# Kernel tuning notes

Measured on AMD Instinct MI355X. Metric: run time of the kernel, lower is better.

Reference implementation:

```python
import jax, jax.numpy as jnp
import numpy as np

WS = 8            # window_size
SHIFT = WS // 2   # cyclic shift for 'SW' type
HEAD_DIM = 32

def _rel_index(ws):
    # pairwise relative coordinate indices within a window, offset to [0, 2ws-2]
    cord = np.array([[i, j] for i in range(ws) for j in range(ws)])
    rel = cord[:, None, :] - cord[None, :, :] + ws - 1
    return rel[:, :, 0], rel[:, :, 1]

def _shift_mask(h_w, w_w, p):
    # boolean attention mask for shifted windows; True = masked (-inf)
    s = p - SHIFT
    m = np.zeros((h_w, w_w, p, p, p, p), dtype=bool)
    m[-1, :, :s, :, s:, :] = True
    m[-1, :, s:, :, :s, :] = True
    m[:, -1, :, :s, :, s:] = True
    m[:, -1, :, s:, :, :s] = True
    return m.reshape(h_w * w_w, p * p, p * p)

def setup_inputs() -> dict:
    key = jax.random.key(0)
    ks = jax.random.split(key, 6)
    b, H, W, c = 4, 256, 256, 256
    nh = c // HEAD_DIM
    return {
        "x": jax.random.normal(ks[0], (b, H, W, c), jnp.float32),
        "W_qkv": jax.random.normal(ks[1], (c, 3 * c), jnp.float32) * 0.02,
        "b_qkv": jnp.zeros((3 * c,), jnp.float32),
        "rel_pos": jax.random.normal(ks[2], (nh, 2 * WS - 1, 2 * WS - 1), jnp.float32) * 0.02,
        "W_out": jax.random.normal(ks[3], (c, c), jnp.float32) * 0.02,
        "b_out": jnp.zeros((c,), jnp.float32),
    }

def reference(x, W_qkv, b_qkv, rel_pos, W_out, b_out):
    b, H, W, c = x.shape
    nh = c // HEAD_DIM
    scale = HEAD_DIM ** -0.5
    # cyclic shift (type == 'SW')
    x = jnp.roll(x, (-SHIFT, -SHIFT), axis=(1, 2))
    hw, ww = H // WS, W // WS
    nw, p2 = hw * ww, WS * WS
    # partition into windows: [b, nw, p2, c]
    xw = x.reshape(b, hw, WS, ww, WS, c).transpose(0, 1, 3, 2, 4, 5).reshape(b, nw, p2, c)
    # QKV projection; layout of out dim is (3, n_heads, head_dim)
    qkv = (xw @ W_qkv + b_qkv).reshape(b, nw, p2, 3, nh, HEAD_DIM)
    q, k, v = qkv[..., 0, :, :], qkv[..., 1, :, :], qkv[..., 2, :, :]
    # attention scores per head/window: [h, b, nw, p2, p2]
    sim = jnp.einsum('bwphc,bwqhc->hbwpq', q, k) * scale
    ri, rj = _rel_index(WS)
    sim = sim + rel_pos[:, ri, rj][:, None, None]            # relative position bias
    mask = jnp.asarray(_shift_mask(hw, ww, WS))              # [nw, p2, p2]
    sim = jnp.where(mask[None, None], -jnp.inf, sim)
    probs = jax.nn.softmax(sim, axis=-1)
    out = jnp.einsum('hbwpq,bwqhc->bwphc', probs, v).reshape(b, nw, p2, nh * HEAD_DIM)
    out = out @ W_out + b_out
    # un-window: [b, H, W, c_out]
    out = out.reshape(b, hw, ww, WS, WS, -1).transpose(0, 1, 3, 2, 4, 5).reshape(b, H, W, -1)
    return jnp.roll(out, (SHIFT, SHIFT), axis=(1, 2))
```

## Files before the change

kernel.cpp:

```cpp
#include <hip/hip_runtime.h>
#include <hip/hip_bf16.h>

typedef __attribute__((ext_vector_type(4))) float f32x4;
typedef __attribute__((ext_vector_type(2))) unsigned int u32x2;
typedef __attribute__((ext_vector_type(8))) short s16x8;
typedef __attribute__((ext_vector_type(8))) __bf16 bf16v8;
typedef __attribute__((ext_vector_type(8))) _Float16 f16v8;

#define LDS_XS 0
#define LDS_QS 32768
#define LDS_KS 65536
#define LDS_VT 98304
#define LDS_PR 131072
#define LDS_TOT 147456

__device__ __forceinline__ f32x4 mfma16(s16x8 a, s16x8 b, f32x4 c) {
  return __builtin_amdgcn_mfma_f32_16x16x32_bf16(
      __builtin_bit_cast(bf16v8, a), __builtin_bit_cast(bf16v8, b), c, 0, 0, 0);
}
__device__ __forceinline__ f32x4 mfma16h(s16x8 a, s16x8 b, f32x4 c) {
  return __builtin_amdgcn_mfma_f32_16x16x32_f16(
      __builtin_bit_cast(f16v8, a), __builtin_bit_cast(f16v8, b), c, 0, 0, 0);
}

__device__ __forceinline__ unsigned int cvt2(float a, float b) {
  __hip_bfloat162 r = __float22bfloat162_rn(make_float2(a, b));
  unsigned int u;
  __builtin_memcpy(&u, &r, 4);
  return u;
}
__device__ __forceinline__ unsigned int cvt2h(float a, float b) {
  auto r = __builtin_amdgcn_cvt_pkrtz(a, b);
  unsigned int u;
  __builtin_memcpy(&u, &r, 4);
  return u;
}

__device__ __forceinline__ short f2bf(float f) {
  unsigned u = __float_as_uint(f);
  u += 0x7fffu + ((u >> 16) & 1u);
  return (short)(u >> 16);
}

__device__ __forceinline__ int swz512(int row, int colByte) {
  return row * 512 + (colByte ^ ((row & 7) << 4));
}
__device__ __forceinline__ int swz128(int row, int colByte) {
  return row * 128 + (colByte ^ ((row & 7) << 4));
}

__global__ void prep_w(const float* __restrict__ Wqkv, const float* __restrict__ Wout,
                       const float* __restrict__ relp,
                       short* __restrict__ wqkvT, short* __restrict__ wH,
                       float* __restrict__ relt) {
  int t = blockIdx.x * 256 + threadIdx.x;
  if (t < 768 * 256) {
    int n = t >> 8, k = t & 255;
    wqkvT[t] = f2bf(Wqkv[k * 768 + n]);
  } else if (t < 768 * 256 + 256 * 256) {
    int t2 = t - 768 * 256;
    int n = t2 >> 8, k = t2 & 255;
    _Float16 h = (_Float16)Wout[k * 256 + n];
    unsigned short us;
    __builtin_memcpy(&us, &h, 2);
    wH[t2] = (short)us;
  } else {
    int u = t - 768 * 256 - 256 * 256;
    int r = u & 3, l = (u >> 2) & 63, strip = (u >> 8) & 3;
    int qt = (u >> 10) & 3, h = (u >> 12) & 7, var = (u >> 15) & 3;
    int p = strip * 16 + (l & 15);
    int q = qt * 16 + ((l >> 4) << 2) + r;
    int pi = p >> 3, pj = p & 7, qi = q >> 3, qj = q & 7;
    bool mrow = (var >> 1) & 1, mcol = var & 1;
    bool mk = (mrow && ((pi < 4) != (qi < 4))) || (mcol && ((pj < 4) != (qj < 4)));
    relt[u] = mk ? -1e30f : relp[h * 225 + (pi - qi + 7) * 15 + (pj - qj + 7)];
  }
}

__global__ __launch_bounds__(512, 2) void swin_mfma(
    const float* __restrict__ x, const float* __restrict__ bqkv,
    const float* __restrict__ bout,
    const short* __restrict__ wqkvT, const short* __restrict__ wH,
    const float* __restrict__ relt, float* __restrict__ out)
{
  __shared__ __align__(16) char lds[LDS_TOT];

  const int tx = threadIdx.x;
  const int w  = tx >> 6;
  const int l  = tx & 63;
  const int g  = l >> 4;
  const int li = l & 15;

  const int b   = blockIdx.x >> 10;
  const int wdw = blockIdx.x & 1023;
  const int wh  = wdw >> 5, wwi = wdw & 31;

  for (int i = 0; i < 8; ++i) {
    int idx = tx + i * 512;
    int p = idx >> 6, c4 = idx & 63;
    int pi = p >> 3, pj = p & 7;
    int sr = (wh * 8 + pi + 4) & 255;
    int sc = (wwi * 8 + pj + 4) & 255;
    f32x4 v = *(const f32x4*)(x + ((((size_t)b * 256 + sr) * 256 + sc) * 256 + c4 * 4));
    u32x2 uu;
    uu.x = cvt2(v[0], v[1]);
    uu.y = cvt2(v[2], v[3]);
    *(u32x2*)(lds + LDS_XS + swz512(p, c4 * 8)) = uu;
  }
  __syncthreads();

  {
    f32x4 acc[6][4];
    #pragma unroll
    for (int j = 0; j < 6; ++j)
      #pragma unroll
      for (int rb = 0; rb < 4; ++rb)
        acc[j][rb] = (f32x4){0.f, 0.f, 0.f, 0.f};

    int ocol[6];
    #pragma unroll
    for (int j = 0; j < 4; ++j) ocol[j] = (w * 4 + j) * 16 + li;
    #pragma unroll
    for (int j = 4; j < 6; ++j) ocol[j] = 512 + (w * 2 + (j - 4)) * 16 + li;

    s16x8 bcur[6], bnext[6];
    #pragma unroll
    for (int j = 0; j < 6; ++j)
      bcur[j] = *(const s16x8*)(wqkvT + (size_t)ocol[j] * 256 + g * 8);

    #pragma unroll
    for (int kk = 0; kk < 8; ++kk) {
      s16x8 a[4];
      #pragma unroll
      for (int rb = 0; rb < 4; ++rb)
        a[rb] = *(const s16x8*)(lds + LDS_XS + swz512(rb * 16 + li, kk * 64 + g * 16));
      if (kk < 7) {
        #pragma unroll
        for (int j = 0; j < 6; ++j)
          bnext[j] = *(const s16x8*)(wqkvT + (size_t)ocol[j] * 256 + (kk + 1) * 32 + g * 8);
      }
      #pragma unroll
      for (int j = 0; j < 4; ++j)
        #pragma unroll
        for (int rb = 0; rb < 4; ++rb)
          acc[j][rb] = mfma16(bcur[j], a[rb], acc[j][rb]);
      #pragma unroll
      for (int j = 4; j < 6; ++j)
        #pragma unroll
        for (int rb = 0; rb < 4; ++rb)
          acc[j][rb] = mfma16(a[rb], bcur[j], acc[j][rb]);
      if (kk < 7) {
        #pragma unroll
        for (int j = 0; j < 6; ++j) bcur[j] = bnext[j];
      }
    }

    #pragma unroll
    for (int j = 0; j < 4; ++j) {
      const int cb = w * 4 + j;
      if (cb < 16) {
        f32x4 bq = *(const f32x4*)(bqkv + cb * 16 + g * 4);
        #pragma unroll
        for (int rb = 0; rb < 4; ++rb) {
          const float SC = 0.17677669529663687f;
          u32x2 uu;
          uu.x = cvt2((acc[j][rb][0] + bq[0]) * SC, (acc[j][rb][1] + bq[1]) * SC);
          uu.y = cvt2((acc[j][rb][2] + bq[2]) * SC, (acc[j][rb][3] + bq[3]) * SC);
          *(u32x2*)(lds + LDS_QS + swz512(rb * 16 + li, cb * 32 + g * 8)) = uu;
        }
      } else {
        f32x4 bk = *(const f32x4*)(bqkv + 256 + (cb - 16) * 16 + g * 4);
        #pragma unroll
        for (int rb = 0; rb < 4; ++rb) {
          u32x2 uu;
          uu.x = cvt2(acc[j][rb][0] + bk[0], acc[j][rb][1] + bk[1]);
          uu.y = cvt2(acc[j][rb][2] + bk[2], acc[j][rb][3] + bk[3]);
          *(u32x2*)(lds + LDS_KS + swz512(rb * 16 + li, (cb - 16) * 32 + g * 8)) = uu;
        }
      }
    }
    #pragma unroll
    for (int j = 4; j < 6; ++j) {
      const int d = (w * 2 + (j - 4)) * 16 + li;
      const float bv = bqkv[512 + d];
      #pragma unroll
      for (int rb = 0; rb < 4; ++rb) {
        u32x2 uu;
        uu.x = cvt2(acc[j][rb][0] + bv, acc[j][rb][1] + bv);
        uu.y = cvt2(acc[j][rb][2] + bv, acc[j][rb][3] + bv);
        *(u32x2*)(lds + LDS_VT + swz128(d, rb * 32 + g * 8)) = uu;
      }
    }
  }
  __syncthreads();

  {
    const int rvar = ((wh == 31) ? 2 : 0) | ((wwi == 31) ? 1 : 0);
    const int hsel = w >> 2, strip = w & 3, p0 = strip * 16;
    const short ONE = (short)0x3F80;
    const s16x8 ones = {ONE, ONE, ONE, ONE, ONE, ONE, ONE, ONE};
    char* prbase = lds + LDS_PR + hsel * 8192;

    #pragma unroll
    for (int hp = 0; hp < 4; ++hp) {
      const int h = hp * 2 + hsel;

      f32x4 rc[4];
      #pragma unroll
      for (int qt = 0; qt < 4; ++qt)
        rc[qt] = *(const f32x4*)(relt + ((((rvar * 8 + h) * 4 + qt) * 4 + strip) * 64 + l) * 4);

      s16x8 qf = *(const s16x8*)(lds + LDS_QS + swz512(p0 + li, h * 64 + g * 16));
      f32x4 simT[4];
      #pragma unroll
      for (int qt = 0; qt < 4; ++qt) {
        s16x8 kf = *(const s16x8*)(lds + LDS_KS + swz512(qt * 16 + li, h * 64 + g * 16));
        simT[qt] = mfma16(kf, qf, rc[qt]);
      }

      #pragma unroll
      for (int qt = 0; qt < 4; ++qt) {
        u32x2 uu;
        uu.x = cvt2(__expf(simT[qt][0]), __expf(simT[qt][1]));
        uu.y = cvt2(__expf(simT[qt][2]), __expf(simT[qt][3]));
        *(u32x2*)(prbase + swz128(p0 + li, qt * 32 + g * 8)) = uu;
      }

      s16x8 pf[2];
      #pragma unroll
      for (int ks = 0; ks < 2; ++ks)
        pf[ks] = *(const s16x8*)(prbase + swz128(p0 + li, ks * 64 + g * 16));

      f32x4 s = (f32x4){0.f, 0.f, 0.f, 0.f};
      f32x4 at0 = (f32x4){0.f, 0.f, 0.f, 0.f};
      f32x4 at1 = (f32x4){0.f, 0.f, 0.f, 0.f};
      #pragma unroll
      for (int ks = 0; ks < 2; ++ks) {
        s = mfma16(ones, pf[ks], s);
        s16x8 vf0 = *(const s16x8*)(lds + LDS_VT + swz128(h * 32 + li, ks * 64 + g * 16));
        s16x8 vf1 = *(const s16x8*)(lds + LDS_VT + swz128(h * 32 + 16 + li, ks * 64 + g * 16));
        at0 = mfma16(vf0, pf[ks], at0);
        at1 = mfma16(vf1, pf[ks], at1);
      }
      const float rinv = 1.0f / s[0];

      #pragma unroll
      for (int dt = 0; dt < 2; ++dt) {
        const f32x4 at = dt ? at1 : at0;
        u32x2 hh;
        hh.x = cvt2h(at[0] * rinv, at[1] * rinv);
        hh.y = cvt2h(at[2] * rinv, at[3] * rinv);
        *(u32x2*)(lds + LDS_XS + swz512(p0 + li, h * 64 + dt * 32 + g * 8)) = hh;
      }
    }
  }
  __syncthreads();

  {
    f32x4 acc2[2][4];
    #pragma unroll
    for (int c = 0; c < 2; ++c)
      #pragma unroll
      for (int rb = 0; rb < 4; ++rb)
        acc2[c][rb] = (f32x4){0.f, 0.f, 0.f, 0.f};

    s16x8 bc[2], bn[2];
    #pragma unroll
    for (int c = 0; c < 2; ++c)
      bc[c] = *(const s16x8*)(wH + (size_t)((w * 2 + c) * 16 + li) * 256 + g * 8);

    #pragma unroll
    for (int kk = 0; kk < 8; ++kk) {
      s16x8 a[4];
      #pragma unroll
      for (int rb = 0; rb < 4; ++rb)
        a[rb] = *(const s16x8*)(lds + LDS_XS + swz512(rb * 16 + li, kk * 64 + g * 16));
      if (kk < 7) {
        #pragma unroll
        for (int c = 0; c < 2; ++c)
          bn[c] = *(const s16x8*)(wH + (size_t)((w * 2 + c) * 16 + li) * 256
                                  + (kk + 1) * 32 + g * 8);
      }
      #pragma unroll
      for (int c = 0; c < 2; ++c)
        #pragma unroll
        for (int rb = 0; rb < 4; ++rb)
          acc2[c][rb] = mfma16h(a[rb], bc[c], acc2[c][rb]);
      if (kk < 7) {
        #pragma unroll
        for (int c = 0; c < 2; ++c) bc[c] = bn[c];
      }
    }

    #pragma unroll
    for (int c = 0; c < 2; ++c) {
      const int n = (w * 2 + c) * 16 + li;
      const float bo = bout[n];
      #pragma unroll
      for (int rb = 0; rb < 4; ++rb)
        #pragma unroll
        for (int r = 0; r < 4; ++r) {
          int m = rb * 16 + g * 4 + r;
          int pi = m >> 3, pj = m & 7;
          int dr = (wh * 8 + pi + 4) & 255;
          int dc = (wwi * 8 + pj + 4) & 255;
          out[(((size_t)b * 256 + dr) * 256 + dc) * 256 + n] = acc2[c][rb][r] + bo;
        }
    }
  }
}

extern "C" void kernel_launch(void* const* d_in, const int* in_sizes, int n_in,
                              void* d_out, int out_size, void* d_ws, size_t ws_size,
                              hipStream_t stream) {
  (void)in_sizes; (void)n_in; (void)out_size; (void)ws_size;
  const float* x    = (const float*)d_in[0];
  const float* Wqkv = (const float*)d_in[1];
  const float* bqkv = (const float*)d_in[2];
  const float* relp = (const float*)d_in[3];
  const float* Wout = (const float*)d_in[4];
  const float* bout = (const float*)d_in[5];
  float* out = (float*)d_out;

  short* wqkvT = (short*)d_ws;
  short* wH    = wqkvT + 768 * 256;
  float* relt  = (float*)(wH + 256 * 256);

  hipLaunchKernelGGL(prep_w, dim3(1536), dim3(256), 0, stream,
                     Wqkv, Wout, relp, wqkvT, wH, relt);
  hipLaunchKernelGGL(swin_mfma, dim3(4096), dim3(512), 0, stream,
                     x, bqkv, bout, wqkvT, wH, relt, out);
}
```

Baseline: 408.6 us.

## Use 1024-thread blocks and keep softmax probabilities in registers

Doubles the block to 16 waves, splitting the QKV projection, per-head attention and output projection across more waves with fewer accumulators each. The attention stage now keeps exponentiated scores in registers as f16 and feeds them straight into a 16x16x16 f16 MFMA against f16 V. This replaces the LDS probability scratch buffer and the ones-vector MFMA row sum with lane shuffles. Dropping the probability buffer shrinks LDS to 128KB and removes an LDS round trip. The trade-offs are a larger block with more barrier participants and f16 instead of bf16 for V and the probabilities.

Result: slower. 457.8 us (+12.0%).

```diff
diff --git a/kernel.cpp b/kernel.cpp
--- a/kernel.cpp
+++ b/kernel.cpp
@@ -6,13 +6,13 @@
 typedef __attribute__((ext_vector_type(8))) short s16x8;
 typedef __attribute__((ext_vector_type(8))) __bf16 bf16v8;
 typedef __attribute__((ext_vector_type(8))) _Float16 f16v8;
+typedef __attribute__((ext_vector_type(4))) _Float16 f16x4;
 
 #define LDS_XS 0
 #define LDS_QS 32768
 #define LDS_KS 65536
 #define LDS_VT 98304
-#define LDS_PR 131072
-#define LDS_TOT 147456
+#define LDS_TOT 131072
 
 __device__ __forceinline__ f32x4 mfma16(s16x8 a, s16x8 b, f32x4 c) {
   return __builtin_amdgcn_mfma_f32_16x16x32_bf16(
@@ -21,6 +21,9 @@
 __device__ __forceinline__ f32x4 mfma16h(s16x8 a, s16x8 b, f32x4 c) {
   return __builtin_amdgcn_mfma_f32_16x16x32_f16(
       __builtin_bit_cast(f16v8, a), __builtin_bit_cast(f16v8, b), c, 0, 0, 0);
+}
+__device__ __forceinline__ f32x4 mfmah16(f16x4 a, f16x4 b, f32x4 c) {
+  return __builtin_amdgcn_mfma_f32_16x16x16f16(a, b, c, 0, 0, 0);
 }
 
 __device__ __forceinline__ unsigned int cvt2(float a, float b) {
@@ -34,6 +37,14 @@
   unsigned int u;
   __builtin_memcpy(&u, &r, 4);
   return u;
+}
+__device__ __forceinline__ f16x4 pack4h(float a, float b, float c, float d) {
+  u32x2 u;
+  u.x = cvt2h(a, b);
+  u.y = cvt2h(c, d);
+  f16x4 r;
+  __builtin_memcpy(&r, &u, 8);
+  return r;
 }
 
 __device__ __forceinline__ short f2bf(float f) {
@@ -77,7 +88,7 @@
   }
 }
 
-__global__ __launch_bounds__(512, 2) void swin_mfma(
+__global__ __launch_bounds__(1024) void swin_mfma(
     const float* __restrict__ x, const float* __restrict__ bqkv,
     const float* __restrict__ bout,
     const short* __restrict__ wqkvT, const short* __restrict__ wH,
@@ -95,8 +106,8 @@
   const int wdw = blockIdx.x & 1023;
   const int wh  = wdw >> 5, wwi = wdw & 31;
 
-  for (int i = 0; i < 8; ++i) {
-    int idx = tx + i * 512;
+  for (int i = 0; i < 4; ++i) {
+    int idx = tx + i * 1024;
     int p = idx >> 6, c4 = idx & 63;
     int pi = p >> 3, pj = p & 7;
     int sr = (wh * 8 + pi + 4) & 255;
@@ -110,23 +121,21 @@
   __syncthreads();
 
   {
-    f32x4 acc[6][4];
-    #pragma unroll
-    for (int j = 0; j < 6; ++j)
+    f32x4 acc[3][4];
+    #pragma unroll
+    for (int j = 0; j < 3; ++j)
       #pragma unroll
       for (int rb = 0; rb < 4; ++rb)
         acc[j][rb] = (f32x4){0.f, 0.f, 0.f, 0.f};
 
-    int ocol[6];
-    #pragma unroll
-    for (int j = 0; j < 4; ++j) ocol[j] = (w * 4 + j) * 16 + li;
-    #pragma unroll
-    for (int j = 4; j < 6; ++j) ocol[j] = 512 + (w * 2 + (j - 4)) * 16 + li;
-
-    s16x8 bcur[6], bnext[6];
-    #pragma unroll
-    for (int j = 0; j < 6; ++j)
-      bcur[j] = *(const s16x8*)(wqkvT + (size_t)ocol[j] * 256 + g * 8);
+    int cb[3];
+    #pragma unroll
+    for (int j = 0; j < 3; ++j) cb[j] = w * 3 + j;
+
+    s16x8 bcur[3], bnext[3];
+    #pragma unroll
+    for (int j = 0; j < 3; ++j)
+      bcur[j] = *(const s16x8*)(wqkvT + (size_t)(cb[j] * 16 + li) * 256 + g * 8);
 
     #pragma unroll
     for (int kk = 0; kk < 8; ++kk) {
@@ -136,59 +145,59 @@
         a[rb] = *(const s16x8*)(lds + LDS_XS + swz512(rb * 16 + li, kk * 64 + g * 16));
       if (kk < 7) {
         #pragma unroll
-        for (int j = 0; j < 6; ++j)
-          bnext[j] = *(const s16x8*)(wqkvT + (size_t)ocol[j] * 256 + (kk + 1) * 32 + g * 8);
-      }
-      #pragma unroll
-      for (int j = 0; j < 4; ++j)
-        #pragma unroll
-        for (int rb = 0; rb < 4; ++rb)
-          acc[j][rb] = mfma16(bcur[j], a[rb], acc[j][rb]);
-      #pragma unroll
-      for (int j = 4; j < 6; ++j)
-        #pragma unroll
-        for (int rb = 0; rb < 4; ++rb)
-          acc[j][rb] = mfma16(a[rb], bcur[j], acc[j][rb]);
+        for (int j = 0; j < 3; ++j)
+          bnext[j] = *(const s16x8*)(wqkvT + (size_t)(cb[j] * 16 + li) * 256
+                                     + (kk + 1) * 32 + g * 8);
+      }
+      #pragma unroll
+      for (int j = 0; j < 3; ++j) {
+        if (cb[j] < 32)
+          #pragma unroll
+          for (int rb = 0; rb < 4; ++rb)
+            acc[j][rb] = mfma16(bcur[j], a[rb], acc[j][rb]);
+        else
+          #pragma unroll
+          for (int rb = 0; rb < 4; ++rb)
+            acc[j][rb] = mfma16(a[rb], bcur[j], acc[j][rb]);
+      }
       if (kk < 7) {
         #pragma unroll
-        for (int j = 0; j < 6; ++j) bcur[j] = bnext[j];
+        for (int j = 0; j < 3; ++j) bcur[j] = bnext[j];
       }
     }
 
     #pragma unroll
-    for (int j = 0; j < 4; ++j) {
-      const int cb = w * 4 + j;
-      if (cb < 16) {
-        f32x4 bq = *(const f32x4*)(bqkv + cb * 16 + g * 4);
+    for (int j = 0; j < 3; ++j) {
+      const int c = cb[j];
+      if (c < 16) {
+        f32x4 bq = *(const f32x4*)(bqkv + c * 16 + g * 4);
         #pragma unroll
         for (int rb = 0; rb < 4; ++rb) {
           const float SC = 0.17677669529663687f;
           u32x2 uu;
           uu.x = cvt2((acc[j][rb][0] + bq[0]) * SC, (acc[j][rb][1] + bq[1]) * SC);
           uu.y = cvt2((acc[j][rb][2] + bq[2]) * SC, (acc[j][rb][3] + bq[3]) * SC);
-          *(u32x2*)(lds + LDS_QS + swz512(rb * 16 + li, cb * 32 + g * 8)) = uu;
+          *(u32x2*)(lds + LDS_QS + swz512(rb * 16 + li, c * 32 + g * 8)) = uu;
         }
-      } else {
-        f32x4 bk = *(const f32x4*)(bqkv + 256 + (cb - 16) * 16 + g * 4);
+      } else if (c < 32) {
+        f32x4 bk = *(const f32x4*)(bqkv + c * 16 + g * 4);
         #pragma unroll
         for (int rb = 0; rb < 4; ++rb) {
           u32x2 uu;
           uu.x = cvt2(acc[j][rb][0] + bk[0], acc[j][rb][1] + bk[1]);
           uu.y = cvt2(acc[j][rb][2] + bk[2], acc[j][rb][3] + bk[3]);
-          *(u32x2*)(lds + LDS_KS + swz512(rb * 16 + li, (cb - 16) * 32 + g * 8)) = uu;
+          *(u32x2*)(lds + LDS_KS + swz512(rb * 16 + li, (c - 16) * 32 + g * 8)) = uu;
         }
-      }
-    }
-    #pragma unroll
-    for (int j = 4; j < 6; ++j) {
-      const int d = (w * 2 + (j - 4)) * 16 + li;
-      const float bv = bqkv[512 + d];
-      #pragma unroll
-      for (int rb = 0; rb < 4; ++rb) {
-        u32x2 uu;
-        uu.x = cvt2(acc[j][rb][0] + bv, acc[j][rb][1] + bv);
-        uu.y = cvt2(acc[j][rb][2] + bv, acc[j][rb][3] + bv);
-        *(u32x2*)(lds + LDS_VT + swz128(d, rb * 32 + g * 8)) = uu;
+      } else {
+        const int d = (c - 32) * 16 + li;
+        const float bv = bqkv[c * 16 + li];
+        #pragma unroll
+        for (int rb = 0; rb < 4; ++rb) {
+          u32x2 uu;
+          uu.x = cvt2h(acc[j][rb][0] + bv, acc[j][rb][1] + bv);
+          uu.y = cvt2h(acc[j][rb][2] + bv, acc[j][rb][3] + bv);
+          *(u32x2*)(lds + LDS_VT + swz128(d, rb * 32 + g * 8)) = uu;
+        }
       }
     }
   }
@@ -196,78 +205,93 @@
 
   {
     const int rvar = ((wh == 31) ? 2 : 0) | ((wwi == 31) ? 1 : 0);
-    const int hsel = w >> 2, strip = w & 3, p0 = strip * 16;
-    const short ONE = (short)0x3F80;
-    const s16x8 ones = {ONE, ONE, ONE, ONE, ONE, ONE, ONE, ONE};
-    char* prbase = lds + LDS_PR + hsel * 8192;
-
-    #pragma unroll
-    for (int hp = 0; hp < 4; ++hp) {
-      const int h = hp * 2 + hsel;
-
-      f32x4 rc[4];
+    const int h = w >> 1, phalf = w & 1, p0 = phalf * 32;
+
+    f32x4 rc[2][4];
+    #pragma unroll
+    for (int pt = 0; pt < 2; ++pt)
       #pragma unroll
       for (int qt = 0; qt < 4; ++qt)
-        rc[qt] = *(const f32x4*)(relt + ((((rvar * 8 + h) * 4 + qt) * 4 + strip) * 64 + l) * 4);
-
-      s16x8 qf = *(const s16x8*)(lds + LDS_QS + swz512(p0 + li, h * 64 + g * 16));
-      f32x4 simT[4];
+        rc[pt][qt] = *(const f32x4*)(relt
+            + ((((rvar * 8 + h) * 4 + qt) * 4 + (phalf * 2 + pt)) * 64 + l) * 4);
+
+    s16x8 qf[2];
+    #pragma unroll
+    for (int pt = 0; pt < 2; ++pt)
+      qf[pt] = *(const s16x8*)(lds + LDS_QS + swz512(p0 + pt * 16 + li, h * 64 + g * 16));
+    s16x8 kf[4];
+    #pragma unroll
+    for (int qt = 0; qt < 4; ++qt)
+      kf[qt] = *(const s16x8*)(lds + LDS_KS + swz512(qt * 16 + li, h * 64 + g * 16));
+    f16x4 vf[2][4];
+    #pragma unroll
+    for (int dt = 0; dt < 2; ++dt)
+      #pragma unroll
+      for (int qt = 0; qt < 4; ++qt)
+        vf[dt][qt] = *(const f16x4*)(lds + LDS_VT
+                                     + swz128(h * 32 + dt * 16 + li, qt * 32 + g * 8));
+
+    f32x4 simT[2][4];
+    #pragma unroll
+    for (int pt = 0; pt < 2; ++pt)
+      #pragma unroll
+      for (int qt = 0; qt < 4; ++qt)
+        simT[pt][qt] = mfma16(kf[qt], qf[pt], rc[pt][qt]);
+
+    float rinv[2];
+    f16x4 pa[2][4];
+    #pragma unroll
+    for (int pt = 0; pt < 2; ++pt) {
+      float s = 0.f;
       #pragma unroll
       for (int qt = 0; qt < 4; ++qt) {
-        s16x8 kf = *(const s16x8*)(lds + LDS_KS + swz512(qt * 16 + li, h * 64 + g * 16));
-        simT[qt] = mfma16(kf, qf, rc[qt]);
-      }
-
-      #pragma unroll
-      for (int qt = 0; qt < 4; ++qt) {
-        u32x2 uu;
-        uu.x = cvt2(__expf(simT[qt][0]), __expf(simT[qt][1]));
-        uu.y = cvt2(__expf(simT[qt][2]), __expf(simT[qt][3]));
-        *(u32x2*)(prbase + swz128(p0 + li, qt * 32 + g * 8)) = uu;
-      }
-
-      s16x8 pf[2];
-      #pragma unroll
-      for (int ks = 0; ks < 2; ++ks)
-        pf[ks] = *(const s16x8*)(prbase + swz128(p0 + li, ks * 64 + g * 16));
-
-      f32x4 s = (f32x4){0.f, 0.f, 0.f, 0.f};
-      f32x4 at0 = (f32x4){0.f, 0.f, 0.f, 0.f};
-      f32x4 at1 = (f32x4){0.f, 0.f, 0.f, 0.f};
-      #pragma unroll
-      for (int ks = 0; ks < 2; ++ks) {
-        s = mfma16(ones, pf[ks], s);
-        s16x8 vf0 = *(const s16x8*)(lds + LDS_VT + swz128(h * 32 + li, ks * 64 + g * 16));
-        s16x8 vf1 = *(const s16x8*)(lds + LDS_VT + swz128(h * 32 + 16 + li, ks * 64 + g * 16));
-        at0 = mfma16(vf0, pf[ks], at0);
-        at1 = mfma16(vf1, pf[ks], at1);
-      }
-      const float rinv = 1.0f / s[0];
-
+        float e0 = __expf(simT[pt][qt][0]);
+        float e1 = __expf(simT[pt][qt][1]);
+        float e2 = __expf(simT[pt][qt][2]);
+        float e3 = __expf(simT[pt][qt][3]);
+        s += (e0 + e1) + (e2 + e3);
+        pa[pt][qt] = pack4h(e0, e1, e2, e3);
+      }
+      s += __shfl_xor(s, 16);
+      s += __shfl_xor(s, 32);
+      rinv[pt] = 1.0f / s;
+    }
+
+    f32x4 at[2][2];
+    #pragma unroll
+    for (int pt = 0; pt < 2; ++pt)
+      #pragma unroll
+      for (int dt = 0; dt < 2; ++dt)
+        at[pt][dt] = (f32x4){0.f, 0.f, 0.f, 0.f};
+    #pragma unroll
+    for (int qt = 0; qt < 4; ++qt)
+      #pragma unroll
+      for (int pt = 0; pt < 2; ++pt)
+        #pragma unroll
+        for (int dt = 0; dt < 2; ++dt)
+          at[pt][dt] = mfmah16(vf[dt][qt], pa[pt][qt], at[pt][dt]);
+
+    #pragma unroll
+    for (int pt = 0; pt < 2; ++pt)
       #pragma unroll
       for (int dt = 0; dt < 2; ++dt) {
-        const f32x4 at = dt ? at1 : at0;
+        const f32x4 a4 = at[pt][dt];
         u32x2 hh;
-        hh.x = cvt2h(at[0] * rinv, at[1] * rinv);
-        hh.y = cvt2h(at[2] * rinv, at[3] * rinv);
-        *(u32x2*)(lds + LDS_XS + swz512(p0 + li, h * 64 + dt * 32 + g * 8)) = hh;
-      }
-    }
+        hh.x = cvt2h(a4[0] * rinv[pt], a4[1] * rinv[pt]);
+        hh.y = cvt2h(a4[2] * rinv[pt], a4[3] * rinv[pt]);
+        *(u32x2*)(lds + LDS_XS + swz512(p0 + pt * 16 + li, h * 64 + dt * 32 + g * 8)) = hh;
+      }
   }
   __syncthreads();
 
   {
-    f32x4 acc2[2][4];
-    #pragma unroll
-    for (int c = 0; c < 2; ++c)
-      #pragma unroll
-      for (int rb = 0; rb < 4; ++rb)
-        acc2[c][rb] = (f32x4){0.f, 0.f, 0.f, 0.f};
-
-    s16x8 bc[2], bn[2];
-    #pragma unroll
-    for (int c = 0; c < 2; ++c)
-      bc[c] = *(const s16x8*)(wH + (size_t)((w * 2 + c) * 16 + li) * 256 + g * 8);
+    f32x4 acc2[4];
+    #pragma unroll
+    for (int rb = 0; rb < 4; ++rb)
+      acc2[rb] = (f32x4){0.f, 0.f, 0.f, 0.f};
+
+    s16x8 bc = *(const s16x8*)(wH + (size_t)(w * 16 + li) * 256 + g * 8);
+    s16x8 bn;
 
     #pragma unroll
     for (int kk = 0; kk < 8; ++kk) {
@@ -275,38 +299,26 @@
       #pragma unroll
       for (int rb = 0; rb < 4; ++rb)
         a[rb] = *(const s16x8*)(lds + LDS_XS + swz512(rb * 16 + li, kk * 64 + g * 16));
-      if (kk < 7) {
-        #pragma unroll
-        for (int c = 0; c < 2; ++c)
-          bn[c] = *(const s16x8*)(wH + (size_t)((w * 2 + c) * 16 + li) * 256
-                                  + (kk + 1) * 32 + g * 8);
-      }
-      #pragma unroll
-      for (int c = 0; c < 2; ++c)
-        #pragma unroll
-        for (int rb = 0; rb < 4; ++rb)
-          acc2[c][rb] = mfma16h(a[rb], bc[c], acc2[c][rb]);
-      if (kk < 7) {
-        #pragma unroll
-        for (int c = 0; c < 2; ++c) bc[c] = bn[c];
-      }
+      if (kk < 7)
+        bn = *(const s16x8*)(wH + (size_t)(w * 16 + li) * 256 + (kk + 1) * 32 + g * 8);
+      #pragma unroll
+      for (int rb = 0; rb < 4; ++rb)
+        acc2[rb] = mfma16h(a[rb], bc, acc2[rb]);
+      if (kk < 7) bc = bn;
     }
 
-    #pragma unroll
-    for (int c = 0; c < 2; ++c) {
-      const int n = (w * 2 + c) * 16 + li;
-      const float bo = bout[n];
-      #pragma unroll
-      for (int rb = 0; rb < 4; ++rb)
-        #pragma unroll
-        for (int r = 0; r < 4; ++r) {
-          int m = rb * 16 + g * 4 + r;
-          int pi = m >> 3, pj = m & 7;
-          int dr = (wh * 8 + pi + 4) & 255;
-          int dc = (wwi * 8 + pj + 4) & 255;
-          out[(((size_t)b * 256 + dr) * 256 + dc) * 256 + n] = acc2[c][rb][r] + bo;
-        }
-    }
+    const int n = w * 16 + li;
+    const float bo = bout[n];
+    #pragma unroll
+    for (int rb = 0; rb < 4; ++rb)
+      #pragma unroll
+      for (int r = 0; r < 4; ++r) {
+        int m = rb * 16 + g * 4 + r;
+        int pi = m >> 3, pj = m & 7;
+        int dr = (wh * 8 + pi + 4) & 255;
+        int dc = (wwi * 8 + pj + 4) & 255;
+        out[(((size_t)b * 256 + dr) * 256 + dc) * 256 + n] = acc2[rb][r] + bo;
+      }
   }
 }
 
@@ -328,6 +340,6 @@
 
   hipLaunchKernelGGL(prep_w, dim3(1536), dim3(256), 0, stream,
                      Wqkv, Wout, relp, wqkvT, wH, relt);
-  hipLaunchKernelGGL(swin_mfma, dim3(4096), dim3(512), 0, stream,
+  hipLaunchKernelGGL(swin_mfma, dim3(4096), dim3(1024), 0, stream,
                      x, bqkv, bout, wqkvT, wH, relt, out);
 }
```
